# Performance work log

Hardware: AMD Instinct MI355X
Metric: run time of the kernel (lower is better)

## Reference

```python
import jax, jax.numpy as jnp
import numpy as np

N = 131072      # total nodes
G = 1024        # graphs
NPG = 128       # nodes per graph (equal-sized graphs, batch sorted)
E = 2097152     # edges (avg degree 16)
H = 64          # hidden_channels
K = 30          # sort-pool k
MAXZ = 1000     # max_z
D = 3 * H + 1   # total_latent_dim = hidden*num_layers + 1 = 193
DENSE = ((K - 2) // 2 + 1 - 5 + 1) * 32  # 352


def setup_inputs():
    key = jax.random.key(0)
    ks = jax.random.split(key, 16)
    z = jax.random.randint(ks[0], (N,), 0, MAXZ)
    # within-graph random edges
    g = jax.random.randint(ks[1], (E,), 0, G)
    src = g * NPG + jax.random.randint(ks[2], (E,), 0, NPG)
    dst = g * NPG + jax.random.randint(ks[3], (E,), 0, NPG)
    edge_index = jnp.stack([src, dst])
    batch = jnp.repeat(jnp.arange(G), NPG)

    def w(k, shape, fan):
        return jax.random.normal(k, shape, dtype=jnp.float32) / np.float32(np.sqrt(fan))

    z_table = w(ks[4], (MAXZ, H), H)
    W0 = w(ks[5], (H, H), H); b0 = jnp.zeros((H,), jnp.float32)
    W1 = w(ks[6], (H, H), H); b1 = jnp.zeros((H,), jnp.float32)
    W2 = w(ks[7], (H, H), H); b2 = jnp.zeros((H,), jnp.float32)
    W3 = w(ks[8], (H, 1), H); b3 = jnp.zeros((1,), jnp.float32)
    conv1_w = w(ks[9], (16, D), D); conv1_b = jnp.zeros((16,), jnp.float32)
    conv2_w = w(ks[10], (32, 16, 5), 16 * 5); conv2_b = jnp.zeros((32,), jnp.float32)
    lin1_w = w(ks[11], (DENSE, 128), DENSE); lin1_b = jnp.zeros((128,), jnp.float32)
    lin2_w = w(ks[12], (128, 1), 128); lin2_b = jnp.zeros((1,), jnp.float32)
    return dict(z=z, edge_index=edge_index, batch=batch, z_table=z_table,
                W0=W0, b0=b0, W1=W1, b1=b1, W2=W2, b2=b2, W3=W3, b3=b3,
                conv1_w=conv1_w, conv1_b=conv1_b, conv2_w=conv2_w, conv2_b=conv2_b,
                lin1_w=lin1_w, lin1_b=lin1_b, lin2_w=lin2_w, lin2_b=lin2_b)


def _forward(z, edge_index, z_table, W0, b0, W1, b1, W2, b2, W3, b3,
             conv1_w, conv1_b, conv2_w, conv2_b, lin1_w, lin1_b, lin2_w, lin2_b):
    src, dst = edge_index[0], edge_index[1]
    loop = jnp.arange(N)
    src_sl = jnp.concatenate([src, loop])  # self-loops (gcn_norm)
    dst_sl = jnp.concatenate([dst, loop])
    deg = jax.ops.segment_sum(jnp.ones((E + N,), jnp.float32), dst_sl, num_segments=N)
    dinv = jnp.where(deg > 0, 1.0 / jnp.sqrt(deg), 0.0)
    norm = dinv[src_sl] * dinv[dst_sl]  # sym-normalized edge weights

    def gcn(x, W, b):
        h = x @ W
        agg = jax.ops.segment_sum(h[src_sl] * norm[:, None], dst_sl, num_segments=N)
        return agg + b

    x = z_table[z]  # z_embedding lookup, [N, H]
    xs = []
    for W, b in ((W0, b0), (W1, b1), (W2, b2), (W3, b3)):
        x = jnp.tanh(gcn(x, W, b))
        xs.append(x)
    xc = jnp.concatenate(xs, axis=-1)  # [N, D] (concat of xs[1:])

    # global_sort_pool: sort per graph by last channel (descending), keep top-K.
    xg = xc.reshape(G, NPG, D)
    order = jnp.argsort(-xg[:, :, -1], axis=1)[:, :K]
    topk = jnp.take_along_axis(xg, order[:, :, None], axis=1)  # [G, K, D]

    # conv1: kernel=stride=D over flattened [G, 1, K*D] == per-node linear D->16
    h1 = jax.nn.relu(jnp.einsum('gkd,cd->gck', topk, conv1_w) + conv1_b[None, :, None])  # [G,16,K]
    p = h1.reshape(G, 16, K // 2, 2).max(-1)  # maxpool1d(2,2) -> [G,16,15]
    h2 = jax.nn.relu(
        jax.lax.conv_general_dilated(p, conv2_w, (1,), 'VALID',
                                     dimension_numbers=('NCH', 'OIH', 'NCH'))
        + conv2_b[None, :, None])  # [G,32,11]
    flat = h2.reshape(G, -1)  # channel-major flatten, matches torch .view
    hm = jax.nn.relu(flat @ lin1_w + lin1_b)  # MLP (dropout off in eval)
    return hm @ lin2_w + lin2_b  # [G, 1]


def reference(z, edge_index, batch, z_table, W0, b0, W1, b1, W2, b2, W3, b3,
              conv1_w, conv1_b, conv2_w, conv2_b, lin1_w, lin1_b, lin2_w, lin2_b):
    del batch  # graphs are equal-sized & node ids contiguous: reshape implements sort-pool segmentation
    return _forward(z, edge_index, z_table, W0, b0, W1, b1, W2, b2, W3, b3,
                    conv1_w, conv1_b, conv2_w, conv2_b, lin1_w, lin1_b, lin2_w, lin2_b)
```

## Files before the change

kernel.cpp:

```cpp
#include <hip/hip_runtime.h>

#define NGRAPH  1024
#define E_EDGES 2097152
#define ECAP    2944
#define MAXZ    1000

__device__ __forceinline__ float bfu_lo(unsigned u) { return __uint_as_float(u << 16); }
__device__ __forceinline__ float bfu_hi(unsigned u) { return __uint_as_float(u & 0xFFFF0000u); }
__device__ __forceinline__ unsigned packlo(float f0, float f1) {
    return (__float_as_uint(f0) >> 16) | (__float_as_uint(f1) & 0xFFFF0000u);
}
__device__ __forceinline__ int xh_idx(int r, int k)  { return (r << 6) | (k  ^ ((r & 7) << 3)); }
__device__ __forceinline__ int xl_idx(int r, int k2) { return (r << 5) | (k2 ^ ((r & 7) << 2)); }

__device__ __forceinline__ double tanh_fast(double p) {
    double q = 2.0 * p;
    q = fmin(40.0, fmax(-40.0, q));
    double nf = rint(q * 1.4426950408889634074);
    double r  = fma(nf, -6.93147180369123816490e-01, q);
    r = fma(nf, -1.90821492927058770002e-10, r);
    double er =     2.755731922398589e-07;
    er = fma(er, r, 2.755731922398589e-06);
    er = fma(er, r, 2.4801587301587302e-05);
    er = fma(er, r, 1.984126984126984e-04);
    er = fma(er, r, 1.3888888888888889e-03);
    er = fma(er, r, 8.333333333333333e-03);
    er = fma(er, r, 4.1666666666666664e-02);
    er = fma(er, r, 1.6666666666666666e-01);
    er = fma(er, r, 0.5);
    er = fma(er, r, 1.0);
    er = fma(er, r, 1.0);
    double E = er * __longlong_as_double((long long)(1023 + (int)nf) << 52);
    return 1.0 - 2.0 / (E + 1.0);
}

__global__ void markWS_kernel(float* out) {
    int i = blockIdx.x * 256 + threadIdx.x;
    if (i < NGRAPH) out[i] = 2.0f;
}

__global__ void adjscatter_kernel(const int* __restrict__ ei,
                                  unsigned* __restrict__ adjG) {
    int e = blockIdx.x * 256 + threadIdx.x;
    if (e >= E_EDGES) return;
    int s = ei[e];
    int d = ei[E_EDGES + e];
    int g = s >> 7;
    int sl = s & 127, dl = d & 127;
    atomicAdd(&adjG[((size_t)g << 12) + (dl << 5) + (sl >> 2)], 1u << ((sl & 3) << 3));
}

__global__ __launch_bounds__(1024, 1) void gnn2_kernel(
    const int* __restrict__ z,
    const unsigned* __restrict__ adjG,
    const float* __restrict__ zt,
    const float* __restrict__ W0, const float* __restrict__ b0,
    const float* __restrict__ W1, const float* __restrict__ b1,
    const float* __restrict__ W2, const float* __restrict__ b2,
    const float* __restrict__ W3, const float* __restrict__ b3,
    const float* __restrict__ c1w, const float* __restrict__ c1b,
    const float* __restrict__ c2w, const float* __restrict__ c2b,
    const float* __restrict__ l1w, const float* __restrict__ l1b,
    const float* __restrict__ l2w, const float* __restrict__ l2b,
    float* __restrict__ xdump,
    float* __restrict__ out)
{
    __shared__ __align__(16) float    Xhi[2][8192];
    __shared__ __align__(16) unsigned Xlo[2][4096];
    __shared__ unsigned char  csr[2][ECAP];
    __shared__ unsigned short rp16[2][132];
    __shared__ int            aux[2][128];
    __shared__ int            inv[2][30];
    __shared__ float          kd30f[2][30];
    __shared__ int            w0tot[2];

    const int half = threadIdx.x >> 9;
    const int tt   = threadIdx.x & 511;
    const int g    = (blockIdx.x << 1) | half;
    const int r0 = tt >> 3;
    const int r1 = r0 + 64;
    const int c0 = (tt & 7) << 3;

    float*          XH = Xhi[half];
    unsigned*       XL = Xlo[half];
    unsigned char*  CS = csr[half];
    unsigned short* RP = rp16[half];
    int*            AX = aux[half];

    unsigned* adjM = (unsigned*)XH;

    {
        const uint4* src = (const uint4*)(adjG + ((size_t)g << 12));
        uint4* dst = (uint4*)adjM;
        for (int i = tt; i < 1024; i += 512) dst[i] = src[i];
    }
    if (tt < 30) { inv[half][tt] = tt; kd30f[half][tt] = 0.f; }
    __syncthreads();

    int degv = 0;
    if (tt < 128) {
        for (int w = 0; w < 32; ++w) {
            unsigned u = adjM[(tt << 5) + w];
            degv += (int)((u & 255u) + ((u >> 8) & 255u) + ((u >> 16) & 255u) + (u >> 24));
        }
        AX[tt] = degv;
    }
    if (tt < 128) {
        int v = degv;
        for (int o = 1; o < 64; o <<= 1) {
            int u = __shfl_up(v, o, 64);
            if ((tt & 63) >= o) v += u;
        }
        if (tt == 63) w0tot[half] = v;
        RP[tt + 1] = (unsigned short)v;
    }
    __syncthreads();
    if (tt >= 64 && tt < 128) RP[tt + 1] = (unsigned short)(RP[tt + 1] + w0tot[half]);
    if (tt == 0) RP[0] = 0;
    __syncthreads();

    const int mydeg = (tt < 128) ? AX[tt] : 0;
    const double dv0 = 1.0 / sqrt((double)(AX[r0] + 1));
    const double dv1 = 1.0 / sqrt((double)(AX[r1] + 1));
    const double dvm = 1.0 / sqrt((double)(mydeg + 1));

    if (tt < 128) {
        unsigned pos = RP[tt];
        for (int w = 0; w < 32; ++w) {
            unsigned u = adjM[(tt << 5) + w];
            while (u) {
                int b2 = (u & 0xFFu) ? 0 : (u & 0xFF00u) ? 1 : (u & 0xFF0000u) ? 2 : 3;
                int m = (int)((u >> (b2 << 3)) & 255u);
                unsigned char sv = (unsigned char)((w << 2) + b2);
                for (int q = 0; q < m; ++q) { if (pos < ECAP) CS[pos] = sv; ++pos; }
                u &= ~(0xFFu << (b2 << 3));
            }
        }
    }
    __syncthreads();

    for (int idx = tt; idx < 8192; idx += 512) {
        int n = idx >> 6, c = idx & 63;
        int zv = z[(g << 7) + n];
        zv = (zv < 0) ? 0 : ((zv >= MAXZ) ? MAXZ - 1 : zv);
        XH[xh_idx(n, c)] = zt[zv * 64 + c];
    }
    __syncthreads();

    for (int layer = 0; layer < 3; ++layer) {
        const float* Wg = (layer == 0) ? W0 : (layer == 1) ? W1 : W2;
        const float* bg = (layer == 0) ? b0 : (layer == 1) ? b1 : b2;
        const bool haslo = (layer != 0);

        double accd0[8], accd1[8]; float accf0[8], accf1[8];
#pragma unroll
        for (int j = 0; j < 8; ++j) { accd0[j] = 0.0; accd1[j] = 0.0; accf0[j] = 0.f; accf1[j] = 0.f; }

        for (int k = 0; k < 64; k += 4) {
            float4 a0 = *(const float4*)&XH[xh_idx(r0, k)];
            float4 a1 = *(const float4*)&XH[xh_idx(r1, k)];
            float x0[4] = {a0.x, a0.y, a0.z, a0.w};
            float x1[4] = {a1.x, a1.y, a1.z, a1.w};
            float l0[4], l1[4];
            if (haslo) {
                uint2 u0 = *(const uint2*)&XL[xl_idx(r0, k >> 1)];
                uint2 u1 = *(const uint2*)&XL[xl_idx(r1, k >> 1)];
                l0[0] = bfu_lo(u0.x); l0[1] = bfu_hi(u0.x); l0[2] = bfu_lo(u0.y); l0[3] = bfu_hi(u0.y);
                l1[0] = bfu_lo(u1.x); l1[1] = bfu_hi(u1.x); l1[2] = bfu_lo(u1.y); l1[3] = bfu_hi(u1.y);
            }
#pragma unroll
            for (int kk = 0; kk < 4; ++kk) {
                const float* wr = Wg + ((k + kk) << 6) + c0;
                float4 wa = *(const float4*)wr;
                float4 wb = *(const float4*)(wr + 4);
                float wf[8] = {wa.x, wa.y, wa.z, wa.w, wb.x, wb.y, wb.z, wb.w};
                double xd0 = (double)x0[kk], xd1 = (double)x1[kk];
#pragma unroll
                for (int j = 0; j < 8; ++j) {
                    double wd = (double)wf[j];
                    accd0[j] = fma(xd0, wd, accd0[j]);
                    accd1[j] = fma(xd1, wd, accd1[j]);
                }
                if (haslo) {
#pragma unroll
                    for (int j = 0; j < 8; ++j) {
                        accf0[j] = fmaf(l0[kk], wf[j], accf0[j]);
                        accf1[j] = fmaf(l1[kk], wf[j], accf1[j]);
                    }
                }
            }
        }
        __syncthreads();

        float hfv[2][8], rsv[2][8];
#pragma unroll
        for (int rw = 0; rw < 2; ++rw) {
            int rr = rw ? r1 : r0;
            double dv = rw ? dv1 : dv0;
#pragma unroll
            for (int j = 0; j < 8; ++j) {
                double acc = rw ? (accd1[j] + (double)accf1[j]) : (accd0[j] + (double)accf0[j]);
                double h = dv * acc;
                float hf = (float)h;
                hfv[rw][j] = hf;
                rsv[rw][j] = (float)(h - (double)hf);
            }
            int bi = xh_idx(rr, c0);
            *(float4*)&XH[bi]     = make_float4(hfv[rw][0], hfv[rw][1], hfv[rw][2], hfv[rw][3]);
            *(float4*)&XH[bi + 4] = make_float4(hfv[rw][4], hfv[rw][5], hfv[rw][6], hfv[rw][7]);
            uint4 lv;
            lv.x = packlo(rsv[rw][0], rsv[rw][1]);
            lv.y = packlo(rsv[rw][2], rsv[rw][3]);
            lv.z = packlo(rsv[rw][4], rsv[rw][5]);
            lv.w = packlo(rsv[rw][6], rsv[rw][7]);
            *(uint4*)&XL[xl_idx(rr, c0 >> 1)] = lv;
        }
        __syncthreads();

        double ad[2][8]; float af[2][8];
#pragma unroll
        for (int rw = 0; rw < 2; ++rw)
#pragma unroll
            for (int j = 0; j < 8; ++j) { ad[rw][j] = (double)hfv[rw][j]; af[rw][j] = rsv[rw][j]; }

#pragma unroll
        for (int rw = 0; rw < 2; ++rw) {
            int rr = rw ? r1 : r0;
            for (unsigned e = RP[rr]; e < RP[rr + 1]; ++e) {
                int s = CS[e];
                int bi = (s << 6) | (c0 ^ ((s & 7) << 3));
                float4 a = *(const float4*)&XH[bi];
                float4 b = *(const float4*)&XH[bi + 4];
                uint4 lu = *(const uint4*)&XL[(s << 5) | ((c0 >> 1) ^ ((s & 7) << 2))];
                ad[rw][0] += (double)a.x; ad[rw][1] += (double)a.y;
                ad[rw][2] += (double)a.z; ad[rw][3] += (double)a.w;
                ad[rw][4] += (double)b.x; ad[rw][5] += (double)b.y;
                ad[rw][6] += (double)b.z; ad[rw][7] += (double)b.w;
                af[rw][0] += bfu_lo(lu.x); af[rw][1] += bfu_hi(lu.x);
                af[rw][2] += bfu_lo(lu.y); af[rw][3] += bfu_hi(lu.y);
                af[rw][4] += bfu_lo(lu.z); af[rw][5] += bfu_hi(lu.z);
                af[rw][6] += bfu_lo(lu.w); af[rw][7] += bfu_hi(lu.w);
            }
        }
        __syncthreads();

#pragma unroll
        for (int rw = 0; rw < 2; ++rw) {
            int rr = rw ? r1 : r0;
            double dv = rw ? dv1 : dv0;
            float vf[8], rs[8];
#pragma unroll
            for (int j = 0; j < 8; ++j) {
                double v = tanh_fast(dv * (ad[rw][j] + (double)af[rw][j]) + (double)bg[c0 + j]);
                float vfl = (float)v;
                vf[j] = vfl;
                rs[j] = (float)(v - (double)vfl);
            }
            int bi = xh_idx(rr, c0);
            *(float4*)&XH[bi]     = make_float4(vf[0], vf[1], vf[2], vf[3]);
            *(float4*)&XH[bi + 4] = make_float4(vf[4], vf[5], vf[6], vf[7]);
            uint4 lv;
            lv.x = packlo(rs[0], rs[1]);
            lv.y = packlo(rs[2], rs[3]);
            lv.z = packlo(rs[4], rs[5]);
            lv.w = packlo(rs[6], rs[7]);
            *(uint4*)&XL[xl_idx(rr, c0 >> 1)] = lv;

            if (layer < 2) {
                float* xd = xdump + (((size_t)g * 2 + layer) << 13) + (rr << 6) + c0;
                *(float4*)xd       = make_float4(vf[0], vf[1], vf[2], vf[3]);
                *(float4*)(xd + 4) = make_float4(vf[4], vf[5], vf[6], vf[7]);
            }
        }
        __syncthreads();
    }

    double* h4sD  = (double*)XL;
    double* keydD = ((double*)XL) + 128;

    double sdreg = 0.0;
    if (tt < 128) {
        double sd = 0.0; float sf = 0.f;
        for (int k = 0; k < 64; k += 4) {
            float4 a = *(const float4*)&XH[xh_idx(tt, k)];
            uint2  u = *(const uint2*)&XL[xl_idx(tt, k >> 1)];
            float4 w = *(const float4*)&W3[k];
            sd = fma((double)a.x, (double)w.x, sd);
            sd = fma((double)a.y, (double)w.y, sd);
            sd = fma((double)a.z, (double)w.z, sd);
            sd = fma((double)a.w, (double)w.w, sd);
            sf = fmaf(bfu_lo(u.x), w.x, sf);
            sf = fmaf(bfu_hi(u.x), w.y, sf);
            sf = fmaf(bfu_lo(u.y), w.z, sf);
            sf = fmaf(bfu_hi(u.y), w.w, sf);
        }
        sdreg = sd + (double)sf;
    }
    __syncthreads();
    if (tt < 128) h4sD[tt] = dvm * sdreg;
    __syncthreads();
    double keyreg = 0.0;
    if (tt < 128) {
        double a = h4sD[tt];
        for (unsigned e = RP[tt]; e < RP[tt + 1]; ++e) a += h4sD[CS[e]];
        keyreg = tanh_fast(dvm * a + (double)b3[0]);
        keydD[tt] = keyreg;
    }
    __syncthreads();

    if (tt < 128) {
        int rk = 0;
        for (int j = 0; j < 128; ++j) {
            double kj = keydD[j];
            if (kj > keyreg || (kj == keyreg && j < tt)) ++rk;
        }
        if (rk < 30) { inv[half][rk] = tt; kd30f[half][rk] = (float)keyreg; }
    }
    __syncthreads();

    float* XloF = (float*)XL;
    float* h1v = XloF + 2560;
    float* ppv = XloF + 3040;
    float* flv = XloF + 3280;
    float* hmv = XloF + 3632;

    if (tt < 480) {
        int c = tt & 15, k = tt >> 4;
        int node = inv[half][k];
        const float* wrow = c1w + c * 193;
        const float* xg0 = xdump + ((size_t)g * 2) * 8192 + node * 64;
        const float* xg1 = xg0 + 8192;
        float s8[8];
#pragma unroll
        for (int cg = 0; cg < 8; ++cg) {
            float acc = 0.f;
            float4 xa = *(const float4*)&xg0[cg * 8];
            float4 xb = *(const float4*)&xg0[cg * 8 + 4];
            const float* w0p = wrow + cg * 8;
            acc = fmaf(xa.x, w0p[0], acc); acc = fmaf(xa.y, w0p[1], acc);
            acc = fmaf(xa.z, w0p[2], acc); acc = fmaf(xa.w, w0p[3], acc);
            acc = fmaf(xb.x, w0p[4], acc); acc = fmaf(xb.y, w0p[5], acc);
            acc = fmaf(xb.z, w0p[6], acc); acc = fmaf(xb.w, w0p[7], acc);
            float4 ya = *(const float4*)&xg1[cg * 8];
            float4 yb = *(const float4*)&xg1[cg * 8 + 4];
            const float* w1p = wrow + 64 + cg * 8;
            acc = fmaf(ya.x, w1p[0], acc); acc = fmaf(ya.y, w1p[1], acc);
            acc = fmaf(ya.z, w1p[2], acc); acc = fmaf(ya.w, w1p[3], acc);
            acc = fmaf(yb.x, w1p[4], acc); acc = fmaf(yb.y, w1p[5], acc);
            acc = fmaf(yb.z, w1p[6], acc); acc = fmaf(yb.w, w1p[7], acc);
            const float* w2p = wrow + 128 + cg * 8;
#pragma unroll
            for (int j = 0; j < 8; ++j)
                acc = fmaf(XH[xh_idx(node, cg * 8 + j)], w2p[j], acc);
            s8[cg] = acc;
        }
        float A0 = s8[0] + s8[1], A1 = s8[2] + s8[3];
        float A2 = s8[4] + s8[5], A3 = s8[6] + s8[7];
        float G = (A0 + A1) + (A2 + A3);
        float s = G + c1w[c * 193 + 192] * kd30f[half][k] + c1b[c];
        h1v[c * 30 + k] = s > 0.f ? s : 0.f;
    }
    __syncthreads();
    if (tt < 240) {
        int c = tt & 15, i = tt >> 4;
        float a = h1v[c * 30 + 2 * i], b = h1v[c * 30 + 2 * i + 1];
        ppv[c * 15 + i] = a > b ? a : b;
    }
    __syncthreads();
    if (tt < 352) {
        int o = tt / 11, j = tt % 11;
        float s = c2b[o];
        for (int i = 0; i < 16; ++i)
#pragma unroll
            for (int u = 0; u < 5; ++u)
                s = fmaf(ppv[i * 15 + j + u], c2w[o * 80 + i * 5 + u], s);
        flv[tt] = s > 0.f ? s : 0.f;
    }
    __syncthreads();
    if (tt < 128) {
        float s = l1b[tt];
        for (int i = 0; i < 352; ++i) s = fmaf(flv[i], l1w[i * 128 + tt], s);
        hmv[tt] = s > 0.f ? s : 0.f;
    }
    __syncthreads();
    if (tt < 64) {
        float v = fmaf(hmv[tt], l2w[tt], hmv[tt + 64] * l2w[tt + 64]);
#pragma unroll
        for (int o = 32; o > 0; o >>= 1) v += __shfl_down(v, o, 64);
        if (tt == 0) out[g] = v + l2b[0];
    }
}

__global__ __launch_bounds__(512, 2) void gnn_kernel(
    const int* __restrict__ z,
    const unsigned* __restrict__ adjG,
    const float* __restrict__ zt,
    const float* __restrict__ W0, const float* __restrict__ b0,
    const float* __restrict__ W1, const float* __restrict__ b1,
    const float* __restrict__ W2, const float* __restrict__ b2,
    const float* __restrict__ W3, const float* __restrict__ b3,
    const float* __restrict__ c1w, const float* __restrict__ c1b,
    const float* __restrict__ c2w, const float* __restrict__ c2b,
    const float* __restrict__ l1w, const float* __restrict__ l1b,
    const float* __restrict__ l2w, const float* __restrict__ l2b,
    float* __restrict__ out)
{
    __shared__ __align__(16) float    Xhi[8192];
    __shared__ __align__(16) unsigned Xlo[4096];
    __shared__ unsigned char  csr[ECAP];
    __shared__ unsigned short rp16[132];
    __shared__ int            aux[128];
    __shared__ int            inv[30];
    __shared__ float          kd30f[30];
    __shared__ int            w0tot;

    const int g  = blockIdx.x;
    const int t  = threadIdx.x;
    const int r0 = t >> 3;
    const int r1 = r0 + 64;
    const int c0 = (t & 7) << 3;

    unsigned* adjM = (unsigned*)Xhi;

    {
        const uint4* src = (const uint4*)(adjG + ((size_t)g << 12));
        uint4* dst = (uint4*)adjM;
        for (int i = t; i < 1024; i += 512) dst[i] = src[i];
    }
    if (t < 30) { inv[t] = t; kd30f[t] = 0.f; }
    __syncthreads();

    int degv = 0;
    if (t < 128) {
        for (int w = 0; w < 32; ++w) {
            unsigned u = adjM[(t << 5) + w];
            degv += (int)((u & 255u) + ((u >> 8) & 255u) + ((u >> 16) & 255u) + (u >> 24));
        }
        aux[t] = degv;
    }
    if (t < 128) {
        int v = degv;
        for (int o = 1; o < 64; o <<= 1) {
            int u = __shfl_up(v, o, 64);
            if ((t & 63) >= o) v += u;
        }
        if (t == 63) w0tot = v;
        rp16[t + 1] = (unsigned short)v;
    }
    __syncthreads();
    if (t >= 64 && t < 128) rp16[t + 1] = (unsigned short)(rp16[t + 1] + w0tot);
    if (t == 0) rp16[0] = 0;
    __syncthreads();

    const int mydeg = (t < 128) ? aux[t] : 0;
    const double dv0 = 1.0 / sqrt((double)(aux[r0] + 1));
    const double dv1 = 1.0 / sqrt((double)(aux[r1] + 1));
    const double dvm = 1.0 / sqrt((double)(mydeg + 1));

    if (t < 128) {
        unsigned pos = rp16[t];
        for (int w = 0; w < 32; ++w) {
            unsigned u = adjM[(t << 5) + w];
            while (u) {
                int b2 = (u & 0xFFu) ? 0 : (u & 0xFF00u) ? 1 : (u & 0xFF0000u) ? 2 : 3;
                int m = (int)((u >> (b2 << 3)) & 255u);
                unsigned char sv = (unsigned char)((w << 2) + b2);
                for (int q = 0; q < m; ++q) { if (pos < ECAP) csr[pos] = sv; ++pos; }
                u &= ~(0xFFu << (b2 << 3));
            }
        }
    }
    __syncthreads();

    for (int idx = t; idx < 8192; idx += 512) {
        int n = idx >> 6, c = idx & 63;
        int zv = z[(g << 7) + n];
        zv = (zv < 0) ? 0 : ((zv >= MAXZ) ? MAXZ - 1 : zv);
        Xhi[xh_idx(n, c)] = zt[zv * 64 + c];
    }
    __syncthreads();

    float g1p[2][16];
#pragma unroll
    for (int rw = 0; rw < 2; ++rw)
#pragma unroll
        for (int c = 0; c < 16; ++c) g1p[rw][c] = 0.f;

    for (int layer = 0; layer < 3; ++layer) {
        const float* Wg = (layer == 0) ? W0 : (layer == 1) ? W1 : W2;
        const float* bg = (layer == 0) ? b0 : (layer == 1) ? b1 : b2;
        const bool haslo = (layer != 0);

        double accd0[8], accd1[8]; float accf0[8], accf1[8];
#pragma unroll
        for (int j = 0; j < 8; ++j) { accd0[j] = 0.0; accd1[j] = 0.0; accf0[j] = 0.f; accf1[j] = 0.f; }

        for (int k = 0; k < 64; k += 4) {
            float4 a0 = *(const float4*)&Xhi[xh_idx(r0, k)];
            float4 a1 = *(const float4*)&Xhi[xh_idx(r1, k)];
            float x0[4] = {a0.x, a0.y, a0.z, a0.w};
            float x1[4] = {a1.x, a1.y, a1.z, a1.w};
            float l0[4], l1[4];
            if (haslo) {
                uint2 u0 = *(const uint2*)&Xlo[xl_idx(r0, k >> 1)];
                uint2 u1 = *(const uint2*)&Xlo[xl_idx(r1, k >> 1)];
                l0[0] = bfu_lo(u0.x); l0[1] = bfu_hi(u0.x); l0[2] = bfu_lo(u0.y); l0[3] = bfu_hi(u0.y);
                l1[0] = bfu_lo(u1.x); l1[1] = bfu_hi(u1.x); l1[2] = bfu_lo(u1.y); l1[3] = bfu_hi(u1.y);
            }
#pragma unroll
            for (int kk = 0; kk < 4; ++kk) {
                const float* wr = Wg + ((k + kk) << 6) + c0;
                float4 wa = *(const float4*)wr;
                float4 wb = *(const float4*)(wr + 4);
                float wf[8] = {wa.x, wa.y, wa.z, wa.w, wb.x, wb.y, wb.z, wb.w};
                double xd0 = (double)x0[kk], xd1 = (double)x1[kk];
#pragma unroll
                for (int j = 0; j < 8; ++j) {
                    double wd = (double)wf[j];
                    accd0[j] = fma(xd0, wd, accd0[j]);
                    accd1[j] = fma(xd1, wd, accd1[j]);
                }
                if (haslo) {
#pragma unroll
                    for (int j = 0; j < 8; ++j) {
                        accf0[j] = fmaf(l0[kk], wf[j], accf0[j]);
                        accf1[j] = fmaf(l1[kk], wf[j], accf1[j]);
                    }
                }
            }
        }
        __syncthreads();

        float hfv[2][8], rsv[2][8];
#pragma unroll
        for (int rw = 0; rw < 2; ++rw) {
            int rr = rw ? r1 : r0;
            double dv = rw ? dv1 : dv0;
#pragma unroll
            for (int j = 0; j < 8; ++j) {
                double acc = rw ? (accd1[j] + (double)accf1[j]) : (accd0[j] + (double)accf0[j]);
                double h = dv * acc;
                float hf = (float)h;
                hfv[rw][j] = hf;
                rsv[rw][j] = (float)(h - (double)hf);
            }
            int bi = xh_idx(rr, c0);
            *(float4*)&Xhi[bi]     = make_float4(hfv[rw][0], hfv[rw][1], hfv[rw][2], hfv[rw][3]);
            *(float4*)&Xhi[bi + 4] = make_float4(hfv[rw][4], hfv[rw][5], hfv[rw][6], hfv[rw][7]);
            uint4 lv;
            lv.x = packlo(rsv[rw][0], rsv[rw][1]);
            lv.y = packlo(rsv[rw][2], rsv[rw][3]);
            lv.z = packlo(rsv[rw][4], rsv[rw][5]);
            lv.w = packlo(rsv[rw][6], rsv[rw][7]);
            *(uint4*)&Xlo[xl_idx(rr, c0 >> 1)] = lv;
        }
        __syncthreads();

        double ad[2][8]; float af[2][8];
#pragma unroll
        for (int rw = 0; rw < 2; ++rw)
#pragma unroll
            for (int j = 0; j < 8; ++j) { ad[rw][j] = (double)hfv[rw][j]; af[rw][j] = rsv[rw][j]; }

#pragma unroll
        for (int rw = 0; rw < 2; ++rw) {
            int rr = rw ? r1 : r0;
            for (unsigned e = rp16[rr]; e < rp16[rr + 1]; ++e) {
                int s = csr[e];
                int bi = (s << 6) | (c0 ^ ((s & 7) << 3));
                float4 a = *(const float4*)&Xhi[bi];
                float4 b = *(const float4*)&Xhi[bi + 4];
                uint4 lu = *(const uint4*)&Xlo[(s << 5) | ((c0 >> 1) ^ ((s & 7) << 2))];
                ad[rw][0] += (double)a.x; ad[rw][1] += (double)a.y;
                ad[rw][2] += (double)a.z; ad[rw][3] += (double)a.w;
                ad[rw][4] += (double)b.x; ad[rw][5] += (double)b.y;
                ad[rw][6] += (double)b.z; ad[rw][7] += (double)b.w;
                af[rw][0] += bfu_lo(lu.x); af[rw][1] += bfu_hi(lu.x);
                af[rw][2] += bfu_lo(lu.y); af[rw][3] += bfu_hi(lu.y);
                af[rw][4] += bfu_lo(lu.z); af[rw][5] += bfu_hi(lu.z);
                af[rw][6] += bfu_lo(lu.w); af[rw][7] += bfu_hi(lu.w);
            }
        }
        __syncthreads();

#pragma unroll
        for (int rw = 0; rw < 2; ++rw) {
            int rr = rw ? r1 : r0;
            double dv = rw ? dv1 : dv0;
            float vf[8], rs[8];
#pragma unroll
            for (int j = 0; j < 8; ++j) {
                double v = tanh_fast(dv * (ad[rw][j] + (double)af[rw][j]) + (double)bg[c0 + j]);
                float vfl = (float)v;
                vf[j] = vfl;
                rs[j] = (float)(v - (double)vfl);
            }
            int bi = xh_idx(rr, c0);
            *(float4*)&Xhi[bi]     = make_float4(vf[0], vf[1], vf[2], vf[3]);
            *(float4*)&Xhi[bi + 4] = make_float4(vf[4], vf[5], vf[6], vf[7]);
            uint4 lv;
            lv.x = packlo(rs[0], rs[1]);
            lv.y = packlo(rs[2], rs[3]);
            lv.z = packlo(rs[4], rs[5]);
            lv.w = packlo(rs[6], rs[7]);
            *(uint4*)&Xlo[xl_idx(rr, c0 >> 1)] = lv;

            const float* w1base = c1w + layer * 64 + c0;
            for (int c = 0; c < 16; ++c) {
                const float* wr = w1base + c * 193;
#pragma unroll
                for (int j = 0; j < 8; ++j)
                    g1p[rw][c] = fmaf(vf[j], wr[j], g1p[rw][c]);
            }
        }
        __syncthreads();
    }

    double* h4sD  = (double*)Xlo;
    double* keydD = ((double*)Xlo) + 128;

    double sdreg = 0.0;
    if (t < 128) {
        double sd = 0.0; float sf = 0.f;
        for (int k = 0; k < 64; k += 4) {
            float4 a = *(const float4*)&Xhi[xh_idx(t, k)];
            uint2  u = *(const uint2*)&Xlo[xl_idx(t, k >> 1)];
            float4 w = *(const float4*)&W3[k];
            sd = fma((double)a.x, (double)w.x, sd);
            sd = fma((double)a.y, (double)w.y, sd);
            sd = fma((double)a.z, (double)w.z, sd);
            sd = fma((double)a.w, (double)w.w, sd);
            sf = fmaf(bfu_lo(u.x), w.x, sf);
            sf = fmaf(bfu_hi(u.x), w.y, sf);
            sf = fmaf(bfu_lo(u.y), w.z, sf);
            sf = fmaf(bfu_hi(u.y), w.w, sf);
        }
        sdreg = sd + (double)sf;
    }
    __syncthreads();
    if (t < 128) h4sD[t] = dvm * sdreg;
    __syncthreads();
    double keyreg = 0.0;
    if (t < 128) {
        double a = h4sD[t];
        for (unsigned e = rp16[t]; e < rp16[t + 1]; ++e) a += h4sD[csr[e]];
        keyreg = tanh_fast(dvm * a + (double)b3[0]);
        keydD[t] = keyreg;
    }
    __syncthreads();

    if (t < 128) {
        int rk = 0;
        for (int j = 0; j < 128; ++j) {
            double kj = keydD[j];
            if (kj > keyreg || (kj == keyreg && j < t)) ++rk;
        }
        if (rk < 30) { inv[rk] = t; kd30f[rk] = (float)keyreg; }
    }

#pragma unroll
    for (int m = 1; m <= 4; m <<= 1) {
#pragma unroll
        for (int rw = 0; rw < 2; ++rw)
#pragma unroll
            for (int c = 0; c < 16; ++c)
                g1p[rw][c] += __shfl_xor(g1p[rw][c], m, 64);
    }
    __syncthreads();
    float* XloF = (float*)Xlo;
    float* G1   = XloF + 512;
    if ((t & 7) == 0) {
#pragma unroll
        for (int c = 0; c < 16; c += 4) {
            *(float4*)&G1[r0 * 16 + c] = make_float4(g1p[0][c], g1p[0][c + 1], g1p[0][c + 2], g1p[0][c + 3]);
            *(float4*)&G1[r1 * 16 + c] = make_float4(g1p[1][c], g1p[1][c + 1], g1p[1][c + 2], g1p[1][c + 3]);
        }
    }
    __syncthreads();

    float* h1v = XloF + 2560;
    float* ppv = XloF + 3040;
    float* flv = XloF + 3280;
    float* hmv = XloF + 3632;

    if (t < 480) {
        int c = t & 15, k = t >> 4;
        int node = inv[k];
        float s = G1[node * 16 + c] + c1w[c * 193 + 192] * kd30f[k] + c1b[c];
        h1v[c * 30 + k] = s > 0.f ? s : 0.f;
    }
    __syncthreads();
    if (t < 240) {
        int c = t & 15, i = t >> 4;
        float a = h1v[c * 30 + 2 * i], b = h1v[c * 30 + 2 * i + 1];
        ppv[c * 15 + i] = a > b ? a : b;
    }
    __syncthreads();
    if (t < 352) {
        int o = t / 11, j = t % 11;
        float s = c2b[o];
        for (int i = 0; i < 16; ++i)
#pragma unroll
            for (int u = 0; u < 5; ++u)
                s = fmaf(ppv[i * 15 + j + u], c2w[o * 80 + i * 5 + u], s);
        flv[t] = s > 0.f ? s : 0.f;
    }
    __syncthreads();
    if (t < 128) {
        float s = l1b[t];
        for (int i = 0; i < 352; ++i) s = fmaf(flv[i], l1w[i * 128 + t], s);
        hmv[t] = s > 0.f ? s : 0.f;
    }
    __syncthreads();
    if (t < 64) {
        float v = fmaf(hmv[t], l2w[t], hmv[t + 64] * l2w[t + 64]);
#pragma unroll
        for (int o = 32; o > 0; o >>= 1) v += __shfl_down(v, o, 64);
        if (t == 0) out[g] = v + l2b[0];
    }
}


extern "C" void kernel_launch(void* const* d_in, const int* in_sizes, int n_in,
                              void* d_out, int out_size, void* d_ws, size_t ws_size,
                              hipStream_t stream) {
    const int*   z   = (const int*)d_in[0];
    const int*   ei  = (const int*)d_in[1];
    const float* zt  = (const float*)d_in[3];
    const float* W0  = (const float*)d_in[4];
    const float* b0  = (const float*)d_in[5];
    const float* W1  = (const float*)d_in[6];
    const float* b1  = (const float*)d_in[7];
    const float* W2  = (const float*)d_in[8];
    const float* b2  = (const float*)d_in[9];
    const float* W3  = (const float*)d_in[10];
    const float* b3  = (const float*)d_in[11];
    const float* c1w = (const float*)d_in[12];
    const float* c1b = (const float*)d_in[13];
    const float* c2w = (const float*)d_in[14];
    const float* c2b = (const float*)d_in[15];
    const float* l1w = (const float*)d_in[16];
    const float* l1b = (const float*)d_in[17];
    const float* l2w = (const float*)d_in[18];
    const float* l2b = (const float*)d_in[19];
    float* out = (float*)d_out;

    const size_t ADJ_B = (size_t)NGRAPH * 4096 * 4;
    const size_t XD_B  = (size_t)NGRAPH * 2 * 8192 * 4;
    if (ws_size < ADJ_B) {
        markWS_kernel<<<4, 256, 0, stream>>>(out);
        return;
    }

    unsigned* adjG = (unsigned*)d_ws;

    hipMemsetAsync(adjG, 0, ADJ_B, stream);
    adjscatter_kernel<<<(E_EDGES + 255) / 256, 256, 0, stream>>>(ei, adjG);

    if (ws_size >= ADJ_B + XD_B) {
        float* xdump = (float*)((char*)d_ws + ADJ_B);
        gnn2_kernel<<<NGRAPH / 2, 1024, 0, stream>>>(z, adjG, zt,
                                                     W0, b0, W1, b1, W2, b2, W3, b3,
                                                     c1w, c1b, c2w, c2b, l1w, l1b, l2w, l2b,
                                                     xdump, out);
    } else {
        gnn_kernel<<<NGRAPH, 512, 0, stream>>>(z, adjG, zt,
                                               W0, b0, W1, b1, W2, b2, W3, b3,
                                               c1w, c1b, c2w, c2b, l1w, l1b, l2w, l2b,
                                               out);
    }
}
```

Baseline: 599.7 us.

## Store node features as full fp64 in LDS instead of fp32 hi + bf16 lo split

Replaces the split fp32+bf16-residual feature storage with plain double-precision features in shared memory, using a new XOR swizzle for double2 access. A small prep kernel converts the layer weights to fp64 once per call so the inner GEMM reads doubles directly instead of converting floats. This removes the split/pack/unpack arithmetic and the second float accumulation chain, and it restructures aggregation to read the transformed features from LDS. In exchange, shared memory per block grows, LDS traffic per element doubles, and an extra kernel launch is added.

```diff
diff --git a/kernel.cpp b/kernel.cpp
--- a/kernel.cpp
+++ b/kernel.cpp
@@ -4,14 +4,11 @@
 #define E_EDGES 2097152
 #define ECAP    2944
 #define MAXZ    1000
-
-__device__ __forceinline__ float bfu_lo(unsigned u) { return __uint_as_float(u << 16); }
-__device__ __forceinline__ float bfu_hi(unsigned u) { return __uint_as_float(u & 0xFFFF0000u); }
-__device__ __forceinline__ unsigned packlo(float f0, float f1) {
-    return (__float_as_uint(f0) >> 16) | (__float_as_uint(f1) & 0xFFFF0000u);
+#define WD_ELEMS 12352
+
+__device__ __forceinline__ int xd_idx(int r, int c) {
+    return (r << 6) | (c ^ ((r & 7) << 1) ^ ((c & 48) >> 3));
 }
-__device__ __forceinline__ int xh_idx(int r, int k)  { return (r << 6) | (k  ^ ((r & 7) << 3)); }
-__device__ __forceinline__ int xl_idx(int r, int k2) { return (r << 5) | (k2 ^ ((r & 7) << 2)); }
 
 __device__ __forceinline__ double tanh_fast(double p) {
     double q = 2.0 * p;
@@ -50,14 +47,23 @@
     atomicAdd(&adjG[((size_t)g << 12) + (dl << 5) + (sl >> 2)], 1u << ((sl & 3) << 3));
 }
 
-__global__ __launch_bounds__(1024, 1) void gnn2_kernel(
+__global__ void wprep_kernel(const float* __restrict__ W0, const float* __restrict__ W1,
+                             const float* __restrict__ W2, const float* __restrict__ W3,
+                             double* __restrict__ Wd) {
+    int i = blockIdx.x * 256 + threadIdx.x;
+    if (i < 4096)       Wd[i] = (double)W0[i];
+    else if (i < 8192)  Wd[i] = (double)W1[i - 4096];
+    else if (i < 12288) Wd[i] = (double)W2[i - 8192];
+    else if (i < WD_ELEMS) Wd[i] = (double)W3[i - 12288];
+}
+
+__global__ __launch_bounds__(1024, 1) void gnnf64_kernel(
     const int* __restrict__ z,
     const unsigned* __restrict__ adjG,
     const float* __restrict__ zt,
-    const float* __restrict__ W0, const float* __restrict__ b0,
-    const float* __restrict__ W1, const float* __restrict__ b1,
-    const float* __restrict__ W2, const float* __restrict__ b2,
-    const float* __restrict__ W3, const float* __restrict__ b3,
+    const double* __restrict__ Wd,
+    const float* __restrict__ b0, const float* __restrict__ b1,
+    const float* __restrict__ b2, const float* __restrict__ b3,
     const float* __restrict__ c1w, const float* __restrict__ c1b,
     const float* __restrict__ c2w, const float* __restrict__ c2b,
     const float* __restrict__ l1w, const float* __restrict__ l1b,
@@ -65,8 +71,10 @@
     float* __restrict__ xdump,
     float* __restrict__ out)
 {
-    __shared__ __align__(16) float    Xhi[2][8192];
-    __shared__ __align__(16) unsigned Xlo[2][4096];
+    __shared__ __align__(16) double Xd[2][8192];
+    __shared__ __align__(16) double h4sD[2][128];
+    __shared__ __align__(16) double keydD[2][128];
+    __shared__ __align__(16) float  hscr[2][1200];
     __shared__ unsigned char  csr[2][ECAP];
     __shared__ unsigned short rp16[2][132];
     __shared__ int            aux[2][128];
@@ -81,13 +89,12 @@
     const int r1 = r0 + 64;
     const int c0 = (tt & 7) << 3;
 
-    float*          XH = Xhi[half];
-    unsigned*       XL = Xlo[half];
+    double*         XD = Xd[half];
     unsigned char*  CS = csr[half];
     unsigned short* RP = rp16[half];
     int*            AX = aux[half];
 
-    unsigned* adjM = (unsigned*)XH;
+    unsigned* adjM = (unsigned*)XD;
 
     {
         const uint4* src = (const uint4*)(adjG + ((size_t)g << 12));
@@ -143,186 +150,148 @@
         int n = idx >> 6, c = idx & 63;
         int zv = z[(g << 7) + n];
         zv = (zv < 0) ? 0 : ((zv >= MAXZ) ? MAXZ - 1 : zv);
-        XH[xh_idx(n, c)] = zt[zv * 64 + c];
+        XD[xd_idx(n, c)] = (double)zt[zv * 64 + c];
     }
     __syncthreads();
 
     for (int layer = 0; layer < 3; ++layer) {
-        const float* Wg = (layer == 0) ? W0 : (layer == 1) ? W1 : W2;
-        const float* bg = (layer == 0) ? b0 : (layer == 1) ? b1 : b2;
-        const bool haslo = (layer != 0);
-
-        double accd0[8], accd1[8]; float accf0[8], accf1[8];
-#pragma unroll
-        for (int j = 0; j < 8; ++j) { accd0[j] = 0.0; accd1[j] = 0.0; accf0[j] = 0.f; accf1[j] = 0.f; }
+        const double* Wg = Wd + (layer << 12);
+        const float*  bg = (layer == 0) ? b0 : (layer == 1) ? b1 : b2;
+
+        double acc0[8], acc1[8];
+#pragma unroll
+        for (int j = 0; j < 8; ++j) { acc0[j] = 0.0; acc1[j] = 0.0; }
 
         for (int k = 0; k < 64; k += 4) {
-            float4 a0 = *(const float4*)&XH[xh_idx(r0, k)];
-            float4 a1 = *(const float4*)&XH[xh_idx(r1, k)];
-            float x0[4] = {a0.x, a0.y, a0.z, a0.w};
-            float x1[4] = {a1.x, a1.y, a1.z, a1.w};
-            float l0[4], l1[4];
-            if (haslo) {
-                uint2 u0 = *(const uint2*)&XL[xl_idx(r0, k >> 1)];
-                uint2 u1 = *(const uint2*)&XL[xl_idx(r1, k >> 1)];
-                l0[0] = bfu_lo(u0.x); l0[1] = bfu_hi(u0.x); l0[2] = bfu_lo(u0.y); l0[3] = bfu_hi(u0.y);
-                l1[0] = bfu_lo(u1.x); l1[1] = bfu_hi(u1.x); l1[2] = bfu_lo(u1.y); l1[3] = bfu_hi(u1.y);
-            }
+            int b0i = (r0 << 6) | (k ^ ((r0 & 7) << 1) ^ ((k & 48) >> 3));
+            int b1i = b0i + 4096;
+            double2 xa = *(const double2*)&XD[b0i];
+            double2 xb = *(const double2*)&XD[b0i ^ 2];
+            double2 ya = *(const double2*)&XD[b1i];
+            double2 yb = *(const double2*)&XD[b1i ^ 2];
+            double x0[4] = {xa.x, xa.y, xb.x, xb.y};
+            double x1[4] = {ya.x, ya.y, yb.x, yb.y};
 #pragma unroll
             for (int kk = 0; kk < 4; ++kk) {
-                const float* wr = Wg + ((k + kk) << 6) + c0;
-                float4 wa = *(const float4*)wr;
-                float4 wb = *(const float4*)(wr + 4);
-                float wf[8] = {wa.x, wa.y, wa.z, wa.w, wb.x, wb.y, wb.z, wb.w};
-                double xd0 = (double)x0[kk], xd1 = (double)x1[kk];
+                const double* wr = Wg + ((k + kk) << 6) + c0;
+                double2 w0v = *(const double2*)wr;
+                double2 w1v = *(const double2*)(wr + 2);
+                double2 w2v = *(const double2*)(wr + 4);
+                double2 w3v = *(const double2*)(wr + 6);
+                double wv[8] = {w0v.x, w0v.y, w1v.x, w1v.y, w2v.x, w2v.y, w3v.x, w3v.y};
 #pragma unroll
                 for (int j = 0; j < 8; ++j) {
-                    double wd = (double)wf[j];
-                    accd0[j] = fma(xd0, wd, accd0[j]);
-                    accd1[j] = fma(xd1, wd, accd1[j]);
+                    acc0[j] = fma(x0[kk], wv[j], acc0[j]);
+                    acc1[j] = fma(x1[kk], wv[j], acc1[j]);
                 }
-                if (haslo) {
-#pragma unroll
-                    for (int j = 0; j < 8; ++j) {
-                        accf0[j] = fmaf(l0[kk], wf[j], accf0[j]);
-                        accf1[j] = fmaf(l1[kk], wf[j], accf1[j]);
-                    }
-                }
             }
         }
         __syncthreads();
 
-        float hfv[2][8], rsv[2][8];
+        {
+            int bi = xd_idx(r0, c0);
+            *(double2*)&Xd[half][bi]     = make_double2(dv0 * acc0[0], dv0 * acc0[1]);
+            *(double2*)&Xd[half][bi ^ 2] = make_double2(dv0 * acc0[2], dv0 * acc0[3]);
+            *(double2*)&Xd[half][bi ^ 4] = make_double2(dv0 * acc0[4], dv0 * acc0[5]);
+            *(double2*)&Xd[half][bi ^ 6] = make_double2(dv0 * acc0[6], dv0 * acc0[7]);
+            int bj = xd_idx(r1, c0);
+            *(double2*)&Xd[half][bj]     = make_double2(dv1 * acc1[0], dv1 * acc1[1]);
+            *(double2*)&Xd[half][bj ^ 2] = make_double2(dv1 * acc1[2], dv1 * acc1[3]);
+            *(double2*)&Xd[half][bj ^ 4] = make_double2(dv1 * acc1[4], dv1 * acc1[5]);
+            *(double2*)&Xd[half][bj ^ 6] = make_double2(dv1 * acc1[6], dv1 * acc1[7]);
+        }
+        __syncthreads();
+
+        double tv[2][8];
 #pragma unroll
         for (int rw = 0; rw < 2; ++rw) {
             int rr = rw ? r1 : r0;
             double dv = rw ? dv1 : dv0;
-#pragma unroll
-            for (int j = 0; j < 8; ++j) {
-                double acc = rw ? (accd1[j] + (double)accf1[j]) : (accd0[j] + (double)accf0[j]);
-                double h = dv * acc;
-                float hf = (float)h;
-                hfv[rw][j] = hf;
-                rsv[rw][j] = (float)(h - (double)hf);
-            }
-            int bi = xh_idx(rr, c0);
-            *(float4*)&XH[bi]     = make_float4(hfv[rw][0], hfv[rw][1], hfv[rw][2], hfv[rw][3]);
-            *(float4*)&XH[bi + 4] = make_float4(hfv[rw][4], hfv[rw][5], hfv[rw][6], hfv[rw][7]);
-            uint4 lv;
-            lv.x = packlo(rsv[rw][0], rsv[rw][1]);
-            lv.y = packlo(rsv[rw][2], rsv[rw][3]);
-            lv.z = packlo(rsv[rw][4], rsv[rw][5]);
-            lv.w = packlo(rsv[rw][6], rsv[rw][7]);
-            *(uint4*)&XL[xl_idx(rr, c0 >> 1)] = lv;
+            int bio = xd_idx(rr, c0);
+            double2 p0 = *(const double2*)&XD[bio];
+            double2 p1 = *(const double2*)&XD[bio ^ 2];
+            double2 p2 = *(const double2*)&XD[bio ^ 4];
+            double2 p3 = *(const double2*)&XD[bio ^ 6];
+            double ad[8];
+            ad[0] = p0.x; ad[1] = p0.y; ad[2] = p1.x; ad[3] = p1.y;
+            ad[4] = p2.x; ad[5] = p2.y; ad[6] = p3.x; ad[7] = p3.y;
+
+            for (unsigned e = RP[rr]; e < RP[rr + 1]; ++e) {
+                int s = CS[e];
+                int bi = (s << 6) | (c0 ^ ((s & 7) << 1) ^ ((c0 & 48) >> 3));
+                double2 q0 = *(const double2*)&XD[bi];
+                double2 q1 = *(const double2*)&XD[bi ^ 2];
+                double2 q2 = *(const double2*)&XD[bi ^ 4];
+                double2 q3 = *(const double2*)&XD[bi ^ 6];
+                ad[0] += q0.x; ad[1] += q0.y;
+                ad[2] += q1.x; ad[3] += q1.y;
+                ad[4] += q2.x; ad[5] += q2.y;
+                ad[6] += q3.x; ad[7] += q3.y;
+            }
+#pragma unroll
+            for (int j = 0; j < 8; ++j)
+                tv[rw][j] = tanh_fast(dv * ad[j] + (double)bg[c0 + j]);
         }
         __syncthreads();
-
-        double ad[2][8]; float af[2][8];
-#pragma unroll
-        for (int rw = 0; rw < 2; ++rw)
-#pragma unroll
-            for (int j = 0; j < 8; ++j) { ad[rw][j] = (double)hfv[rw][j]; af[rw][j] = rsv[rw][j]; }
 
 #pragma unroll
         for (int rw = 0; rw < 2; ++rw) {
             int rr = rw ? r1 : r0;
-            for (unsigned e = RP[rr]; e < RP[rr + 1]; ++e) {
-                int s = CS[e];
-                int bi = (s << 6) | (c0 ^ ((s & 7) << 3));
-                float4 a = *(const float4*)&XH[bi];
-                float4 b = *(const float4*)&XH[bi + 4];
-                uint4 lu = *(const uint4*)&XL[(s << 5) | ((c0 >> 1) ^ ((s & 7) << 2))];
-                ad[rw][0] += (double)a.x; ad[rw][1] += (double)a.y;
-                ad[rw][2] += (double)a.z; ad[rw][3] += (double)a.w;
-                ad[rw][4] += (double)b.x; ad[rw][5] += (double)b.y;
-                ad[rw][6] += (double)b.z; ad[rw][7] += (double)b.w;
-                af[rw][0] += bfu_lo(lu.x); af[rw][1] += bfu_hi(lu.x);
-                af[rw][2] += bfu_lo(lu.y); af[rw][3] += bfu_hi(lu.y);
-                af[rw][4] += bfu_lo(lu.z); af[rw][5] += bfu_hi(lu.z);
-                af[rw][6] += bfu_lo(lu.w); af[rw][7] += bfu_hi(lu.w);
-            }
-        }
-        __syncthreads();
-
-#pragma unroll
-        for (int rw = 0; rw < 2; ++rw) {
-            int rr = rw ? r1 : r0;
-            double dv = rw ? dv1 : dv0;
-            float vf[8], rs[8];
-#pragma unroll
-            for (int j = 0; j < 8; ++j) {
-                double v = tanh_fast(dv * (ad[rw][j] + (double)af[rw][j]) + (double)bg[c0 + j]);
-                float vfl = (float)v;
-                vf[j] = vfl;
-                rs[j] = (float)(v - (double)vfl);
-            }
-            int bi = xh_idx(rr, c0);
-            *(float4*)&XH[bi]     = make_float4(vf[0], vf[1], vf[2], vf[3]);
-            *(float4*)&XH[bi + 4] = make_float4(vf[4], vf[5], vf[6], vf[7]);
-            uint4 lv;
-            lv.x = packlo(rs[0], rs[1]);
-            lv.y = packlo(rs[2], rs[3]);
-            lv.z = packlo(rs[4], rs[5]);
-            lv.w = packlo(rs[6], rs[7]);
-            *(uint4*)&XL[xl_idx(rr, c0 >> 1)] = lv;
+            int bi = xd_idx(rr, c0);
+            *(double2*)&XD[bi]     = make_double2(tv[rw][0], tv[rw][1]);
+            *(double2*)&XD[bi ^ 2] = make_double2(tv[rw][2], tv[rw][3]);
+            *(double2*)&XD[bi ^ 4] = make_double2(tv[rw][4], tv[rw][5]);
+            *(double2*)&XD[bi ^ 6] = make_double2(tv[rw][6], tv[rw][7]);
 
             if (layer < 2) {
                 float* xd = xdump + (((size_t)g * 2 + layer) << 13) + (rr << 6) + c0;
-                *(float4*)xd       = make_float4(vf[0], vf[1], vf[2], vf[3]);
-                *(float4*)(xd + 4) = make_float4(vf[4], vf[5], vf[6], vf[7]);
+                *(float4*)xd       = make_float4((float)tv[rw][0], (float)tv[rw][1],
+                                                 (float)tv[rw][2], (float)tv[rw][3]);
+                *(float4*)(xd + 4) = make_float4((float)tv[rw][4], (float)tv[rw][5],
+                                                 (float)tv[rw][6], (float)tv[rw][7]);
             }
         }
         __syncthreads();
     }
-
-    double* h4sD  = (double*)XL;
-    double* keydD = ((double*)XL) + 128;
 
     double sdreg = 0.0;
     if (tt < 128) {
-        double sd = 0.0; float sf = 0.f;
-        for (int k = 0; k < 64; k += 4) {
-            float4 a = *(const float4*)&XH[xh_idx(tt, k)];
-            uint2  u = *(const uint2*)&XL[xl_idx(tt, k >> 1)];
-            float4 w = *(const float4*)&W3[k];
-            sd = fma((double)a.x, (double)w.x, sd);
-            sd = fma((double)a.y, (double)w.y, sd);
-            sd = fma((double)a.z, (double)w.z, sd);
-            sd = fma((double)a.w, (double)w.w, sd);
-            sf = fmaf(bfu_lo(u.x), w.x, sf);
-            sf = fmaf(bfu_hi(u.x), w.y, sf);
-            sf = fmaf(bfu_lo(u.y), w.z, sf);
-            sf = fmaf(bfu_hi(u.y), w.w, sf);
-        }
-        sdreg = sd + (double)sf;
-    }
-    __syncthreads();
-    if (tt < 128) h4sD[tt] = dvm * sdreg;
+        const double* W3d = Wd + 12288;
+        double sd = 0.0;
+        for (int k = 0; k < 64; k += 2) {
+            int bi = (tt << 6) | (k ^ ((tt & 7) << 1) ^ ((k & 48) >> 3));
+            double2 a = *(const double2*)&XD[bi];
+            double2 w = *(const double2*)&W3d[k];
+            sd = fma(a.x, w.x, sd);
+            sd = fma(a.y, w.y, sd);
+        }
+        sdreg = sd;
+    }
+    if (tt < 128) h4sD[half][tt] = dvm * sdreg;
     __syncthreads();
     double keyreg = 0.0;
     if (tt < 128) {
-        double a = h4sD[tt];
-        for (unsigned e = RP[tt]; e < RP[tt + 1]; ++e) a += h4sD[CS[e]];
+        double a = h4sD[half][tt];
+        for (unsigned e = RP[tt]; e < RP[tt + 1]; ++e) a += h4sD[half][CS[e]];
         keyreg = tanh_fast(dvm * a + (double)b3[0]);
-        keydD[tt] = keyreg;
+        keydD[half][tt] = keyreg;
     }
     __syncthreads();
 
     if (tt < 128) {
         int rk = 0;
         for (int j = 0; j < 128; ++j) {
-            double kj = keydD[j];
+            double kj = keydD[half][j];
             if (kj > keyreg || (kj == keyreg && j < tt)) ++rk;
         }
         if (rk < 30) { inv[half][rk] = tt; kd30f[half][rk] = (float)keyreg; }
     }
     __syncthreads();
 
-    float* XloF = (float*)XL;
-    float* h1v = XloF + 2560;
-    float* ppv = XloF + 3040;
-    float* flv = XloF + 3280;
-    float* hmv = XloF + 3632;
+    float* h1v = hscr[half];
+    float* ppv = hscr[half] + 480;
+    float* flv = hscr[half] + 720;
+    float* hmv = hscr[half] + 1072;
 
     if (tt < 480) {
         int c = tt & 15, k = tt >> 4;
@@ -351,7 +320,7 @@
             const float* w2p = wrow + 128 + cg * 8;
 #pragma unroll
             for (int j = 0; j < 8; ++j)
-                acc = fmaf(XH[xh_idx(node, cg * 8 + j)], w2p[j], acc);
+                acc = fmaf((float)XD[xd_idx(node, cg * 8 + j)], w2p[j], acc);
             s8[cg] = acc;
         }
         float A0 = s8[0] + s8[1], A1 = s8[2] + s8[3];
@@ -419,6 +388,14 @@
     const int r0 = t >> 3;
     const int r1 = r0 + 64;
     const int c0 = (t & 7) << 3;
+
+    auto bfu_lo = [](unsigned u) { return __uint_as_float(u << 16); };
+    auto bfu_hi = [](unsigned u) { return __uint_as_float(u & 0xFFFF0000u); };
+    auto packlo = [](float f0, float f1) {
+        return (__float_as_uint(f0) >> 16) | (__float_as_uint(f1) & 0xFFFF0000u);
+    };
+    auto xh_idx = [](int r, int k)  { return (r << 6) | (k  ^ ((r & 7) << 3)); };
+    auto xl_idx = [](int r, int k2) { return (r << 5) | (k2 ^ ((r & 7) << 2)); };
 
     unsigned* adjM = (unsigned*)Xhi;
 
@@ -747,6 +724,7 @@
 
     const size_t ADJ_B = (size_t)NGRAPH * 4096 * 4;
     const size_t XD_B  = (size_t)NGRAPH * 2 * 8192 * 4;
+    const size_t WD_B  = (size_t)WD_ELEMS * 8;
     if (ws_size < ADJ_B) {
         markWS_kernel<<<4, 256, 0, stream>>>(out);
         return;
@@ -757,12 +735,15 @@
     hipMemsetAsync(adjG, 0, ADJ_B, stream);
     adjscatter_kernel<<<(E_EDGES + 255) / 256, 256, 0, stream>>>(ei, adjG);
 
-    if (ws_size >= ADJ_B + XD_B) {
-        float* xdump = (float*)((char*)d_ws + ADJ_B);
-        gnn2_kernel<<<NGRAPH / 2, 1024, 0, stream>>>(z, adjG, zt,
-                                                     W0, b0, W1, b1, W2, b2, W3, b3,
-                                                     c1w, c1b, c2w, c2b, l1w, l1b, l2w, l2b,
-                                                     xdump, out);
+    if (ws_size >= ADJ_B + XD_B + WD_B) {
+        float*  xdump = (float*)((char*)d_ws + ADJ_B);
+        double* Wd    = (double*)((char*)d_ws + ADJ_B + XD_B);
+        wprep_kernel<<<(WD_ELEMS + 255) / 256, 256, 0, stream>>>(W0, W1, W2, W3, Wd);
+        gnnf64_kernel<<<NGRAPH / 2, 1024, 0, stream>>>(z, adjG, zt, Wd,
+                                                       b0, b1, b2, b3,
+                                                       c1w, c1b, c2w, c2b,
+                                                       l1w, l1b, l2w, l2b,
+                                                       xdump, out);
     } else {
         gnn_kernel<<<NGRAPH, 512, 0, stream>>>(z, adjG, zt,
                                                W0, b0, W1, b1, W2, b2, W3, b3,
```

After: 773.7 us. +29.0%, slower.
